# Optimization experiments

Hardware: AMD Instinct MI355X
Metric: run time of the kernel (lower is better)

The kernel has to match this reference:

```python
import jax, jax.numpy as jnp
import numpy as np

B, L, H, NH, NB = 8, 200, 128, 4, 2
HD = H // NH
ITEM_NUM, TIME_SPAN = 50000, 256
PAD = -2.0**32 + 1.0


def setup_inputs() -> dict:
    key = jax.random.key(0)
    ks = jax.random.split(key, 32)
    def g(i, shape, s=0.02):
        return jax.random.normal(ks[i], shape, jnp.float32) * s
    item_emb = g(0, (ITEM_NUM + 1, H)).at[0].set(0.0)  # padding_idx=0
    return dict(
        user_ids=jax.random.randint(ks[1], (B,), 0, 1000),
        log_seqs=jax.random.randint(ks[2], (B, L), 0, ITEM_NUM),
        time_matrices=jax.random.randint(ks[3], (B, L, L), 0, TIME_SPAN + 1),
        pos_seqs=jax.random.randint(ks[4], (B, L), 0, ITEM_NUM + 1),
        neg_seqs=jax.random.randint(ks[5], (B, L), 0, ITEM_NUM + 1),
        item_emb=item_emb,
        pos_K_emb=g(6, (L, H)), pos_V_emb=g(7, (L, H)),
        time_K_emb=g(8, (TIME_SPAN + 1, H)), time_V_emb=g(9, (TIME_SPAN + 1, H)),
        attn_ln_g=jnp.ones((NB, H)), attn_ln_b=jnp.zeros((NB, H)),
        Wq=g(10, (NB, H, H)), bq=jnp.zeros((NB, H)),
        Wk=g(11, (NB, H, H)), bk=jnp.zeros((NB, H)),
        Wv=g(12, (NB, H, H)), bv=jnp.zeros((NB, H)),
        fwd_ln_g=jnp.ones((NB, H)), fwd_ln_b=jnp.zeros((NB, H)),
        W1=g(13, (NB, H, H)), b1=jnp.zeros((NB, H)),
        W2=g(14, (NB, H, H)), b2=jnp.zeros((NB, H)),
        last_ln_g=jnp.ones((H,)), last_ln_b=jnp.zeros((H,)),
    )


def _ln(x, g, b, eps=1e-8):
    m = x.mean(-1, keepdims=True)
    v = jnp.var(x, axis=-1, keepdims=True)
    return (x - m) / jnp.sqrt(v + eps) * g + b


def _heads(x):
    # [..., H] -> [NH, ..., HD]; matches torch.cat(torch.split(x, HD, -1), 0)
    y = x.reshape(x.shape[:-1] + (NH, HD))
    return jnp.moveaxis(y, -2, 0)


def reference(user_ids, log_seqs, time_matrices, pos_seqs, neg_seqs, item_emb,
              pos_K_emb, pos_V_emb, time_K_emb, time_V_emb,
              attn_ln_g, attn_ln_b, Wq, bq, Wk, bk, Wv, bv,
              fwd_ln_g, fwd_ln_b, W1, b1, W2, b2, last_ln_g, last_ln_b):
    # user_ids is unused in the original forward as well.
    tmask = log_seqs == 0                                  # [B,L] True = pad
    keep = (~tmask)[..., None].astype(jnp.float32)
    seqs = item_emb[log_seqs] * np.float32(np.sqrt(H))
    seqs = seqs * keep
    pKh = _heads(pos_K_emb)                                # [NH,L,HD]
    pVh = _heads(pos_V_emb)
    tKh = _heads(time_K_emb[time_matrices])                # [NH,B,L,L,HD]
    tVh = _heads(time_V_emb[time_matrices])
    causal = ~jnp.tril(jnp.ones((L, L), bool))             # True above diag -> masked
    bad = tmask[:, :, None] | causal[None]                 # [B,L,L]
    scale = np.float32(np.sqrt(HD))
    for i in range(NB):
        Qin = _ln(seqs, attn_ln_g[i], attn_ln_b[i])
        Qh = _heads(Qin @ Wq[i].T + bq[i])                 # [NH,B,L,HD]
        Kh = _heads(seqs @ Wk[i].T + bk[i])
        Vh = _heads(seqs @ Wv[i].T + bv[i])
        attn = (jnp.einsum('nbqd,nbkd->nbqk', Qh, Kh)
                + jnp.einsum('nbqd,nkd->nbqk', Qh, pKh)
                + jnp.einsum('nbqkd,nbqd->nbqk', tKh, Qh)) / scale
        attn = jnp.where(bad[None], PAD, attn)
        attn = jax.nn.softmax(attn, axis=-1)
        out = (jnp.einsum('nbqk,nbkd->nbqd', attn, Vh)
               + jnp.einsum('nbqk,nkd->nbqd', attn, pVh)
               + jnp.einsum('nbqk,nbqkd->nbqd', attn, tVh))
        out = jnp.moveaxis(out, 0, -2).reshape(seqs.shape)  # merge heads -> [B,L,H]
        seqs = Qin + out                                    # residual uses LN'd Q (as in source)
        seqs = _ln(seqs, fwd_ln_g[i], fwd_ln_b[i])
        ff = jax.nn.relu(seqs @ W1[i].T + b1[i]) @ W2[i].T + b2[i] + seqs
        seqs = ff * keep
    log_feats = _ln(seqs, last_ln_g, last_ln_b)
    pos_logits = (log_feats * item_emb[pos_seqs]).sum(-1)   # [B,L]
    neg_logits = (log_feats * item_emb[neg_seqs]).sum(-1)
    return pos_logits, neg_logits
```

## Files before the change

kernel.cpp:

```cpp
#include <hip/hip_runtime.h>
#include <hip/hip_bf16.h>

#define BB 8
#define LL 200
#define HH 128
#define NHEAD 4
#define HDIM 32
#define NBLK 2
#define BL (BB * LL)
#define NT 257
#define QT 8
#define NQT 25
#define SSP 208
#define KTP 66
#define TSP 132

static constexpr float SQRT_H    = 11.313708498984761f;
static constexpr float INV_SCALE = 0.17677669529663687f;
static constexpr float PADV      = -4294967295.0f;

__global__ void k_qkv_gemm(const float* __restrict__ seqs_in,
                           const int* __restrict__ log_seqs,
                           const float* __restrict__ item_emb,
                           const float* __restrict__ g, const float* __restrict__ bia,
                           const float* __restrict__ Wq, const float* __restrict__ bq,
                           const float* __restrict__ Wk, const float* __restrict__ bk,
                           const float* __restrict__ Wv, const float* __restrict__ bv,
                           const float* __restrict__ posK, const float* __restrict__ posV,
                           float* __restrict__ Qin, float* __restrict__ Q,
                           float* __restrict__ K, float* __restrict__ V) {
    int mt = blockIdx.x / 24, nt = blockIdx.x % 24;
    int matsel = nt >> 3;
    int jb = (nt & 7) * 16;
    int row0 = mt * 32;
    int tid = threadIdx.x;
    __shared__ float As[32 * TSP];
    __shared__ float Bs[16 * TSP];

    {
        int r = tid >> 3, seg = tid & 7;
        int row = row0 + r;
        float4 vv[4];
        if (seqs_in) {
            #pragma unroll
            for (int i = 0; i < 4; i++)
                vv[i] = *(const float4*)(seqs_in + (size_t)row * HH + seg * 16 + i * 4);
        } else {
            int idx = log_seqs[row];
            if (idx == 0) {
                #pragma unroll
                for (int i = 0; i < 4; i++) vv[i] = make_float4(0.f, 0.f, 0.f, 0.f);
            } else {
                #pragma unroll
                for (int i = 0; i < 4; i++) {
                    float4 e = *(const float4*)(item_emb + (size_t)idx * HH + seg * 16 + i * 4);
                    vv[i] = make_float4(e.x * SQRT_H, e.y * SQRT_H, e.z * SQRT_H, e.w * SQRT_H);
                }
            }
        }
        if (matsel == 0) {
            float s = 0.f, s2 = 0.f;
            #pragma unroll
            for (int i = 0; i < 4; i++) {
                s  += vv[i].x + vv[i].y + vv[i].z + vv[i].w;
                s2 += vv[i].x * vv[i].x + vv[i].y * vv[i].y + vv[i].z * vv[i].z + vv[i].w * vv[i].w;
            }
            #pragma unroll
            for (int off = 1; off < 8; off <<= 1) {
                s  += __shfl_xor(s, off);
                s2 += __shfl_xor(s2, off);
            }
            float mean = s * (1.f / HH);
            float var  = s2 * (1.f / HH) - mean * mean;
            float inv  = 1.f / sqrtf(var + 1e-8f);
            #pragma unroll
            for (int i = 0; i < 4; i++) {
                int k = seg * 16 + i * 4;
                float4 g4 = *(const float4*)(g + k);
                float4 b4 = *(const float4*)(bia + k);
                float4 y;
                y.x = (vv[i].x - mean) * inv * g4.x + b4.x;
                y.y = (vv[i].y - mean) * inv * g4.y + b4.y;
                y.z = (vv[i].z - mean) * inv * g4.z + b4.z;
                y.w = (vv[i].w - mean) * inv * g4.w + b4.w;
                *(float4*)&As[r * TSP + k] = y;
                if (nt == 0) *(float4*)(Qin + (size_t)row * HH + k) = y;
            }
        } else {
            #pragma unroll
            for (int i = 0; i < 4; i++)
                *(float4*)&As[r * TSP + seg * 16 + i * 4] = vv[i];
        }
    }
    {
        const float* W = (matsel == 0) ? Wq : (matsel == 1) ? Wk : Wv;
        int j = tid >> 4, seg = tid & 15;
        float4 w = *(const float4*)(W + (size_t)(jb + j) * HH + seg * 8);
        float4 w2 = *(const float4*)(W + (size_t)(jb + j) * HH + seg * 8 + 4);
        *(float4*)&Bs[j * TSP + seg * 8] = w;
        *(float4*)&Bs[j * TSP + seg * 8 + 4] = w2;
    }
    __syncthreads();

    int m = tid >> 3, jg = tid & 7;
    float acc0 = 0.f, acc1 = 0.f;
    const float* ar = &As[m * TSP];
    const float* b0r = &Bs[(jg * 2) * TSP];
    const float* b1r = &Bs[(jg * 2 + 1) * TSP];
    #pragma unroll 4
    for (int k4 = 0; k4 < 32; k4++) {
        float4 a = *(const float4*)(ar + k4 * 4);
        float4 b0 = *(const float4*)(b0r + k4 * 4);
        float4 b1 = *(const float4*)(b1r + k4 * 4);
        acc0 += a.x * b0.x + a.y * b0.y + a.z * b0.z + a.w * b0.w;
        acc1 += a.x * b1.x + a.y * b1.y + a.z * b1.z + a.w * b1.w;
    }
    int row = row0 + m;
    int col = jb + jg * 2;
    int l = row % LL;
    if (matsel == 0) {
        float2 bb = *(const float2*)(bq + col);
        *(float2*)(Q + (size_t)row * HH + col) =
            make_float2((acc0 + bb.x) * INV_SCALE, (acc1 + bb.y) * INV_SCALE);
    } else if (matsel == 1) {
        float2 bb = *(const float2*)(bk + col);
        float2 pk = *(const float2*)(posK + (size_t)l * HH + col);
        *(float2*)(K + (size_t)row * HH + col) =
            make_float2(acc0 + bb.x + pk.x, acc1 + bb.y + pk.y);
    } else {
        float2 bb = *(const float2*)(bv + col);
        float2 pv = *(const float2*)(posV + (size_t)l * HH + col);
        *(float2*)(V + (size_t)row * HH + col) =
            make_float2(acc0 + bb.x + pv.x, acc1 + bb.y + pv.y);
    }
}

__global__ void k_attn(const float* __restrict__ Q, const float* __restrict__ K,
                       const float* __restrict__ V,
                       const float* __restrict__ timeK, const float* __restrict__ timeV,
                       const int* __restrict__ tm,
                       float* __restrict__ att) {
    int bn = blockIdx.x & 31;
    int b = bn >> 2, n = bn & 3;
    int qt = (NQT - 1) - (blockIdx.x >> 5);
    int q0 = qt * QT;
    int kmax = q0 + QT - 1;
    int tid = threadIdx.x;
    int wv = tid >> 6, ln = tid & 63;

    __shared__ float Qs[QT * HDIM];
    __shared__ float KstT[HDIM * KTP];
    __shared__ float DTW[QT * NT];
    __shared__ float Ssc[QT * SSP];
    __shared__ int   tmst[QT * LL];
    __shared__ float Ost[QT * HDIM];

    Ost[tid] = 0.f;
    if (tid < 64) {
        int qi = tid >> 3, d4 = tid & 7;
        *(float4*)(Qs + qi * HDIM + d4 * 4) =
            *(const float4*)(Q + ((size_t)(b * LL + q0 + qi)) * HH + n * HDIM + d4 * 4);
    }
    #pragma unroll
    for (int qi = 0; qi < QT; qi++)
        if (tid < LL)
            tmst[qi * LL + tid] = tm[((size_t)(b * LL + q0 + qi)) * LL + tid];
    __syncthreads();

    int k2 = tid & 31, qi_c = tid >> 5;

    for (int c = 0; c < 5; c++) {
        #pragma unroll
        for (int p = 0; p < 2; p++) {
            int idx = tid + p * 256;
            int r = idx >> 3, d4 = idx & 7;
            int tau = c * 64 + r;
            float4 w = make_float4(0.f, 0.f, 0.f, 0.f);
            if (tau < NT) w = *(const float4*)(timeK + (size_t)tau * HH + n * HDIM + d4 * 4);
            KstT[(d4 * 4 + 0) * KTP + r] = w.x;
            KstT[(d4 * 4 + 1) * KTP + r] = w.y;
            KstT[(d4 * 4 + 2) * KTP + r] = w.z;
            KstT[(d4 * 4 + 3) * KTP + r] = w.w;
        }
        __syncthreads();
        float a0 = 0.f, a1 = 0.f;
        #pragma unroll 4
        for (int d = 0; d < HDIM; d++) {
            float qv = Qs[qi_c * HDIM + d];
            float2 kv = *(const float2*)&KstT[d * KTP + k2 * 2];
            a0 += qv * kv.x; a1 += qv * kv.y;
        }
        int tau0 = c * 64 + k2 * 2;
        if (tau0 < NT)     DTW[qi_c * NT + tau0]     = a0;
        if (tau0 + 1 < NT) DTW[qi_c * NT + tau0 + 1] = a1;
        __syncthreads();
    }

    int nch = (kmax >> 6) + 1;
    for (int c = 0; c < nch; c++) {
        #pragma unroll
        for (int p = 0; p < 2; p++) {
            int idx = tid + p * 256;
            int r = idx >> 3, d4 = idx & 7;
            int k = c * 64 + r;
            float4 w = make_float4(0.f, 0.f, 0.f, 0.f);
            if (k < LL) w = *(const float4*)(K + ((size_t)(b * LL + k)) * HH + n * HDIM + d4 * 4);
            KstT[(d4 * 4 + 0) * KTP + r] = w.x;
            KstT[(d4 * 4 + 1) * KTP + r] = w.y;
            KstT[(d4 * 4 + 2) * KTP + r] = w.z;
            KstT[(d4 * 4 + 3) * KTP + r] = w.w;
        }
        __syncthreads();
        float a0 = 0.f, a1 = 0.f;
        #pragma unroll 4
        for (int d = 0; d < HDIM; d++) {
            float qv = Qs[qi_c * HDIM + d];
            float2 kv = *(const float2*)&KstT[d * KTP + k2 * 2];
            a0 += qv * kv.x; a1 += qv * kv.y;
        }
        int q = q0 + qi_c;
        int k0 = c * 64 + k2 * 2;
        if (k0 <= kmax)
            Ssc[qi_c * SSP + k0] = (k0 <= q) ? (a0 + DTW[qi_c * NT + tmst[qi_c * LL + k0]]) : PADV;
        if (k0 + 1 <= kmax)
            Ssc[qi_c * SSP + k0 + 1] = (k0 + 1 <= q) ? (a1 + DTW[qi_c * NT + tmst[qi_c * LL + k0 + 1]]) : PADV;
        __syncthreads();
    }

    for (int idx = tid; idx < QT * NT; idx += 256) DTW[idx] = 0.f;
    __syncthreads();

    for (int rr = 0; rr < 2; rr++) {
        int qi = wv + rr * 4;
        int q = q0 + qi;
        float sv[4];
        float m = PADV;
        #pragma unroll
        for (int jj = 0; jj < 4; jj++) {
            int k = ln + 64 * jj;
            sv[jj] = (k <= q) ? Ssc[qi * SSP + k] : PADV;
            m = fmaxf(m, sv[jj]);
        }
        for (int off = 32; off; off >>= 1) m = fmaxf(m, __shfl_xor(m, off));
        float sum = 0.f;
        #pragma unroll
        for (int jj = 0; jj < 4; jj++) {
            int k = ln + 64 * jj;
            sv[jj] = (k <= q) ? __expf(sv[jj] - m) : 0.f;
            sum += sv[jj];
        }
        for (int off = 32; off; off >>= 1) sum += __shfl_xor(sum, off);
        float inv = 1.f / sum;
        #pragma unroll
        for (int jj = 0; jj < 4; jj++) {
            int k = ln + 64 * jj;
            float p = sv[jj] * inv;
            if (k < SSP) Ssc[qi * SSP + k] = (k <= q) ? p : 0.f;
            if (k <= q) atomicAdd(&DTW[qi * NT + tmst[qi * LL + k]], p);
        }
    }
    __syncthreads();

    int d = tid & 31, kg = tid >> 5;
    float acc[QT] = {0,0,0,0,0,0,0,0};
    const float* vb = V + ((size_t)(b * LL)) * HH + n * HDIM + d;
    for (int k = kg; k <= kmax; k += 8) {
        float v = vb[(size_t)k * HH];
        #pragma unroll
        for (int qi = 0; qi < QT; qi++) acc[qi] += Ssc[qi * SSP + k] * v;
    }
    const float* tvb = timeV + n * HDIM + d;
    for (int t = kg; t < NT; t += 8) {
        float v = tvb[(size_t)t * HH];
        #pragma unroll
        for (int qi = 0; qi < QT; qi++) acc[qi] += DTW[qi * NT + t] * v;
    }
    #pragma unroll
    for (int qi = 0; qi < QT; qi++) atomicAdd(&Ost[qi * HDIM + d], acc[qi]);
    __syncthreads();
    {
        int qi = tid >> 5;
        att[((size_t)(b * LL + q0 + qi)) * HH + n * HDIM + (tid & 31)] = Ost[tid];
    }
}

__global__ void k_ff1(const float* __restrict__ Qin, const float* __restrict__ att,
                      const float* __restrict__ g, const float* __restrict__ bia,
                      const float* __restrict__ W1, const float* __restrict__ b1,
                      float* __restrict__ h1) {
    int mt = blockIdx.x >> 3, jb = (blockIdx.x & 7) * 16;
    int row0 = mt * 16;
    int tid = threadIdx.x;
    __shared__ float As[16 * TSP];
    __shared__ float Bs[16 * TSP];

    {
        int r = tid >> 4, seg = tid & 15;
        int row = row0 + r;
        float4 vv[2];
        #pragma unroll
        for (int i = 0; i < 2; i++) {
            int k = seg * 8 + i * 4;
            float4 q4 = *(const float4*)(Qin + (size_t)row * HH + k);
            float4 a4 = *(const float4*)(att + (size_t)row * HH + k);
            vv[i] = make_float4(q4.x + a4.x, q4.y + a4.y, q4.z + a4.z, q4.w + a4.w);
        }
        float s = 0.f, s2 = 0.f;
        #pragma unroll
        for (int i = 0; i < 2; i++) {
            s  += vv[i].x + vv[i].y + vv[i].z + vv[i].w;
            s2 += vv[i].x * vv[i].x + vv[i].y * vv[i].y + vv[i].z * vv[i].z + vv[i].w * vv[i].w;
        }
        #pragma unroll
        for (int off = 1; off < 16; off <<= 1) {
            s  += __shfl_xor(s, off);
            s2 += __shfl_xor(s2, off);
        }
        float mean = s * (1.f / HH);
        float var  = s2 * (1.f / HH) - mean * mean;
        float inv  = 1.f / sqrtf(var + 1e-8f);
        #pragma unroll
        for (int i = 0; i < 2; i++) {
            int k = seg * 8 + i * 4;
            float4 g4 = *(const float4*)(g + k);
            float4 b4 = *(const float4*)(bia + k);
            float4 y;
            y.x = (vv[i].x - mean) * inv * g4.x + b4.x;
            y.y = (vv[i].y - mean) * inv * g4.y + b4.y;
            y.z = (vv[i].z - mean) * inv * g4.z + b4.z;
            y.w = (vv[i].w - mean) * inv * g4.w + b4.w;
            *(float4*)&As[r * TSP + k] = y;
        }
    }
    {
        int j = tid >> 4, seg = tid & 15;
        *(float4*)&Bs[j * TSP + seg * 8]     = *(const float4*)(W1 + (size_t)(jb + j) * HH + seg * 8);
        *(float4*)&Bs[j * TSP + seg * 8 + 4] = *(const float4*)(W1 + (size_t)(jb + j) * HH + seg * 8 + 4);
    }
    __syncthreads();

    int m = tid >> 4, j = tid & 15;
    float acc = 0.f;
    const float* ar = &As[m * TSP];
    const float* br = &Bs[j * TSP];
    #pragma unroll 4
    for (int k4 = 0; k4 < 32; k4++) {
        float4 a = *(const float4*)(ar + k4 * 4);
        float4 b = *(const float4*)(br + k4 * 4);
        acc += a.x * b.x + a.y * b.y + a.z * b.z + a.w * b.w;
    }
    int col = jb + j;
    float t = acc + b1[col];
    h1[(size_t)(row0 + m) * HH + col] = t > 0.f ? t : 0.f;
}

__global__ void k_ff2(const float* __restrict__ h1,
                      const float* __restrict__ Qin, const float* __restrict__ att,
                      const float* __restrict__ g, const float* __restrict__ bia,
                      const float* __restrict__ W2, const float* __restrict__ b2,
                      const int* __restrict__ log_seqs,
                      float* __restrict__ out) {
    int mt = blockIdx.x >> 3, jb = (blockIdx.x & 7) * 16;
    int row0 = mt * 16;
    int tid = threadIdx.x;
    __shared__ float As[16 * TSP];
    __shared__ float Bs[16 * TSP];
    __shared__ float mu[16], rstd[16];

    {
        int r = tid >> 4, seg = tid & 15;
        int row = row0 + r;
        #pragma unroll
        for (int i = 0; i < 2; i++) {
            int k = seg * 8 + i * 4;
            *(float4*)&As[r * TSP + k] = *(const float4*)(h1 + (size_t)row * HH + k);
        }
        float s = 0.f, s2 = 0.f;
        #pragma unroll
        for (int i = 0; i < 2; i++) {
            int k = seg * 8 + i * 4;
            float4 q4 = *(const float4*)(Qin + (size_t)row * HH + k);
            float4 a4 = *(const float4*)(att + (size_t)row * HH + k);
            float4 v = make_float4(q4.x + a4.x, q4.y + a4.y, q4.z + a4.z, q4.w + a4.w);
            s  += v.x + v.y + v.z + v.w;
            s2 += v.x * v.x + v.y * v.y + v.z * v.z + v.w * v.w;
        }
        #pragma unroll
        for (int off = 1; off < 16; off <<= 1) {
            s  += __shfl_xor(s, off);
            s2 += __shfl_xor(s2, off);
        }
        float mean = s * (1.f / HH);
        float var  = s2 * (1.f / HH) - mean * mean;
        if (seg == 0) { mu[r] = mean; rstd[r] = 1.f / sqrtf(var + 1e-8f); }
    }
    {
        int j = tid >> 4, seg = tid & 15;
        *(float4*)&Bs[j * TSP + seg * 8]     = *(const float4*)(W2 + (size_t)(jb + j) * HH + seg * 8);
        *(float4*)&Bs[j * TSP + seg * 8 + 4] = *(const float4*)(W2 + (size_t)(jb + j) * HH + seg * 8 + 4);
    }
    __syncthreads();

    int m = tid >> 4, j = tid & 15;
    float acc = 0.f;
    const float* ar = &As[m * TSP];
    const float* br = &Bs[j * TSP];
    #pragma unroll 4
    for (int k4 = 0; k4 < 32; k4++) {
        float4 a = *(const float4*)(ar + k4 * 4);
        float4 b = *(const float4*)(br + k4 * 4);
        acc += a.x * b.x + a.y * b.y + a.z * b.z + a.w * b.w;
    }
    int row = row0 + m;
    int col = jb + j;
    float resid = Qin[(size_t)row * HH + col] + att[(size_t)row * HH + col];
    float y = (resid - mu[m]) * rstd[m] * g[col] + bia[col];
    float o = acc + b2[col] + y;
    if (log_seqs[row] == 0) o = 0.f;
    out[(size_t)row * HH + col] = o;
}

__global__ void k_lnlogits(const float* __restrict__ seqs,
                           const float* __restrict__ g, const float* __restrict__ bia,
                           const float* __restrict__ item_emb,
                           const int* __restrict__ pos, const int* __restrict__ neg,
                           float* __restrict__ out) {
    int row = blockIdx.x;
    int h = threadIdx.x;
    float v = seqs[(size_t)row * HH + h];
    float s = v, s2 = v * v;
    for (int off = 32; off; off >>= 1) {
        s  += __shfl_xor(s, off);
        s2 += __shfl_xor(s2, off);
    }
    __shared__ float r1[2], r2[2];
    if ((h & 63) == 0) { r1[h >> 6] = s; r2[h >> 6] = s2; }
    __syncthreads();
    float mean = (r1[0] + r1[1]) * (1.f / HH);
    float var  = (r2[0] + r2[1]) * (1.f / HH) - mean * mean;
    float inv = 1.f / sqrtf(var + 1e-8f);
    float f = (v - mean) * inv * g[h] + bia[h];

    int ip = pos[row], in_ = neg[row];
    float vp = f * item_emb[(size_t)ip * HH + h];
    float vn = f * item_emb[(size_t)in_ * HH + h];
    for (int off = 32; off; off >>= 1) {
        vp += __shfl_xor(vp, off);
        vn += __shfl_xor(vn, off);
    }
    __shared__ float rp[2], rn[2];
    if ((h & 63) == 0) { rp[h >> 6] = vp; rn[h >> 6] = vn; }
    __syncthreads();
    if (h == 0) {
        out[row]      = rp[0] + rp[1];
        out[BL + row] = rn[0] + rn[1];
    }
}

extern "C" void kernel_launch(void* const* d_in, const int* in_sizes, int n_in,
                              void* d_out, int out_size, void* d_ws, size_t ws_size,
                              hipStream_t stream) {
    const int* log_seqs   = (const int*)d_in[1];
    const int* tm         = (const int*)d_in[2];
    const int* pos_seqs   = (const int*)d_in[3];
    const int* neg_seqs   = (const int*)d_in[4];
    const float* item_emb = (const float*)d_in[5];
    const float* posK     = (const float*)d_in[6];
    const float* posV     = (const float*)d_in[7];
    const float* timeK    = (const float*)d_in[8];
    const float* timeV    = (const float*)d_in[9];
    const float* attn_g   = (const float*)d_in[10];
    const float* attn_b   = (const float*)d_in[11];
    const float* Wq       = (const float*)d_in[12];
    const float* bq       = (const float*)d_in[13];
    const float* Wk       = (const float*)d_in[14];
    const float* bk       = (const float*)d_in[15];
    const float* Wv       = (const float*)d_in[16];
    const float* bv       = (const float*)d_in[17];
    const float* fwd_g    = (const float*)d_in[18];
    const float* fwd_b    = (const float*)d_in[19];
    const float* W1       = (const float*)d_in[20];
    const float* b1       = (const float*)d_in[21];
    const float* W2       = (const float*)d_in[22];
    const float* b2       = (const float*)d_in[23];
    const float* last_g   = (const float*)d_in[24];
    const float* last_b   = (const float*)d_in[25];

    float* seqs = (float*)d_ws;
    float* Qin  = seqs + (size_t)BL * HH;
    float* Qb   = Qin  + (size_t)BL * HH;
    float* Kb   = Qb   + (size_t)BL * HH;
    float* Vb   = Kb   + (size_t)BL * HH;
    float* att  = Vb   + (size_t)BL * HH;
    float* h1   = att  + (size_t)BL * HH;

    for (int i = 0; i < NBLK; i++) {
        k_qkv_gemm<<<1200, 256, 0, stream>>>(i == 0 ? nullptr : seqs, log_seqs, item_emb,
                                             attn_g + i * HH, attn_b + i * HH,
                                             Wq + (size_t)i * HH * HH, bq + i * HH,
                                             Wk + (size_t)i * HH * HH, bk + i * HH,
                                             Wv + (size_t)i * HH * HH, bv + i * HH,
                                             posK, posV, Qin, Qb, Kb, Vb);
        k_attn<<<NQT * 32, 256, 0, stream>>>(Qb, Kb, Vb, timeK, timeV, tm, att);
        k_ff1<<<800, 256, 0, stream>>>(Qin, att, fwd_g + i * HH, fwd_b + i * HH,
                                       W1 + (size_t)i * HH * HH, b1 + i * HH, h1);
        k_ff2<<<800, 256, 0, stream>>>(h1, Qin, att, fwd_g + i * HH, fwd_b + i * HH,
                                       W2 + (size_t)i * HH * HH, b2 + i * HH,
                                       log_seqs, seqs);
    }
    k_lnlogits<<<BL, HH, 0, stream>>>(seqs, last_g, last_b, item_emb,
                                      pos_seqs, neg_seqs, (float*)d_out);
}
```

Baseline: 235.1 us.

## Fuse all stages into one persistent cooperative kernel with grid syncs

Replaces the nine separate kernel launches with a single persistent cooperative kernel that loops over tiles of each stage and separates stages with grid-wide barriers. Stage bodies become device functions sharing one static shared-memory buffer, and the final layernorm/logits stage handles two rows per block. The aim is to remove inter-kernel launch gaps and tail drain. The cost is grid-sync latency, a larger fixed shared-memory footprint that may limit occupancy, and grid-stride load imbalance (e.g. 1200 qkv tiles over a capped grid). The old multi-kernel path is kept as a fallback if the cooperative launch fails.

```diff
diff --git a/kernel.cpp b/kernel.cpp
--- a/kernel.cpp
+++ b/kernel.cpp
@@ -1,5 +1,7 @@
 #include <hip/hip_runtime.h>
-#include <hip/hip_bf16.h>
+#include <hip/hip_cooperative_groups.h>
+
+namespace cg = cooperative_groups;
 
 #define BB 8
 #define LL 200
@@ -19,23 +21,46 @@
 static constexpr float INV_SCALE = 0.17677669529663687f;
 static constexpr float PADV      = -4294967295.0f;
 
-__global__ void k_qkv_gemm(const float* __restrict__ seqs_in,
-                           const int* __restrict__ log_seqs,
-                           const float* __restrict__ item_emb,
-                           const float* __restrict__ g, const float* __restrict__ bia,
-                           const float* __restrict__ Wq, const float* __restrict__ bq,
-                           const float* __restrict__ Wk, const float* __restrict__ bk,
-                           const float* __restrict__ Wv, const float* __restrict__ bv,
-                           const float* __restrict__ posK, const float* __restrict__ posV,
-                           float* __restrict__ Qin, float* __restrict__ Q,
-                           float* __restrict__ K, float* __restrict__ V) {
-    int mt = blockIdx.x / 24, nt = blockIdx.x % 24;
+#define SMEM_WORDS 8192
+
+struct MegaArgs {
+    const int*   log_seqs;
+    const int*   tm;
+    const int*   pos_seqs;
+    const int*   neg_seqs;
+    const float* item_emb;
+    const float* posK;
+    const float* posV;
+    const float* timeK;
+    const float* timeV;
+    const float* attn_g; const float* attn_b;
+    const float* Wq; const float* bq;
+    const float* Wk; const float* bk;
+    const float* Wv; const float* bv;
+    const float* fwd_g; const float* fwd_b;
+    const float* W1; const float* b1;
+    const float* W2; const float* b2;
+    const float* last_g; const float* last_b;
+    float* seqs; float* Qin; float* Q; float* K; float* V; float* att; float* h1;
+    float* out;
+};
+
+__device__ __forceinline__ void qkv_tile(float* smem, int tile, int tid,
+        const float* seqs_in, const int* __restrict__ log_seqs,
+        const float* __restrict__ item_emb,
+        const float* __restrict__ g, const float* __restrict__ bia,
+        const float* __restrict__ Wq, const float* __restrict__ bq,
+        const float* __restrict__ Wk, const float* __restrict__ bk,
+        const float* __restrict__ Wv, const float* __restrict__ bv,
+        const float* __restrict__ posK, const float* __restrict__ posV,
+        float* __restrict__ Qin, float* __restrict__ Q,
+        float* __restrict__ K, float* __restrict__ V) {
+    float* As = smem;
+    float* Bs = smem + 32 * TSP;
+    int mt = tile / 24, nt = tile % 24;
     int matsel = nt >> 3;
     int jb = (nt & 7) * 16;
     int row0 = mt * 32;
-    int tid = threadIdx.x;
-    __shared__ float As[32 * TSP];
-    __shared__ float Bs[16 * TSP];
 
     {
         int r = tid >> 3, seg = tid & 7;
@@ -95,21 +120,21 @@
     {
         const float* W = (matsel == 0) ? Wq : (matsel == 1) ? Wk : Wv;
         int j = tid >> 4, seg = tid & 15;
-        float4 w = *(const float4*)(W + (size_t)(jb + j) * HH + seg * 8);
+        float4 w  = *(const float4*)(W + (size_t)(jb + j) * HH + seg * 8);
         float4 w2 = *(const float4*)(W + (size_t)(jb + j) * HH + seg * 8 + 4);
-        *(float4*)&Bs[j * TSP + seg * 8] = w;
+        *(float4*)&Bs[j * TSP + seg * 8]     = w;
         *(float4*)&Bs[j * TSP + seg * 8 + 4] = w2;
     }
     __syncthreads();
 
     int m = tid >> 3, jg = tid & 7;
     float acc0 = 0.f, acc1 = 0.f;
-    const float* ar = &As[m * TSP];
+    const float* ar  = &As[m * TSP];
     const float* b0r = &Bs[(jg * 2) * TSP];
     const float* b1r = &Bs[(jg * 2 + 1) * TSP];
     #pragma unroll 4
     for (int k4 = 0; k4 < 32; k4++) {
-        float4 a = *(const float4*)(ar + k4 * 4);
+        float4 a  = *(const float4*)(ar + k4 * 4);
         float4 b0 = *(const float4*)(b0r + k4 * 4);
         float4 b1 = *(const float4*)(b1r + k4 * 4);
         acc0 += a.x * b0.x + a.y * b0.y + a.z * b0.z + a.w * b0.w;
@@ -135,25 +160,24 @@
     }
 }
 
-__global__ void k_attn(const float* __restrict__ Q, const float* __restrict__ K,
-                       const float* __restrict__ V,
-                       const float* __restrict__ timeK, const float* __restrict__ timeV,
-                       const int* __restrict__ tm,
-                       float* __restrict__ att) {
-    int bn = blockIdx.x & 31;
+__device__ __forceinline__ void attn_tile(float* smem, int tile, int tid,
+        const float* __restrict__ Q, const float* __restrict__ K,
+        const float* __restrict__ V,
+        const float* __restrict__ timeK, const float* __restrict__ timeV,
+        const int* __restrict__ tm, float* __restrict__ att) {
+    float* Qs   = smem;
+    float* KstT = smem + 256;
+    float* DTW  = KstT + 2112;
+    float* Ssc  = DTW + 2056;
+    float* Ost  = Ssc + 1664;
+    int*   tmst = (int*)(Ost + 256);
+
+    int bn = tile & 31;
     int b = bn >> 2, n = bn & 3;
-    int qt = (NQT - 1) - (blockIdx.x >> 5);
+    int qt = (NQT - 1) - (tile >> 5);
     int q0 = qt * QT;
     int kmax = q0 + QT - 1;
-    int tid = threadIdx.x;
     int wv = tid >> 6, ln = tid & 63;
-
-    __shared__ float Qs[QT * HDIM];
-    __shared__ float KstT[HDIM * KTP];
-    __shared__ float DTW[QT * NT];
-    __shared__ float Ssc[QT * SSP];
-    __shared__ int   tmst[QT * LL];
-    __shared__ float Ost[QT * HDIM];
 
     Ost[tid] = 0.f;
     if (tid < 64) {
@@ -284,15 +308,15 @@
     }
 }
 
-__global__ void k_ff1(const float* __restrict__ Qin, const float* __restrict__ att,
-                      const float* __restrict__ g, const float* __restrict__ bia,
-                      const float* __restrict__ W1, const float* __restrict__ b1,
-                      float* __restrict__ h1) {
-    int mt = blockIdx.x >> 3, jb = (blockIdx.x & 7) * 16;
+__device__ __forceinline__ void ff1_tile(float* smem, int tile, int tid,
+        const float* __restrict__ Qin, const float* __restrict__ att,
+        const float* __restrict__ g, const float* __restrict__ bia,
+        const float* __restrict__ W1, const float* __restrict__ b1,
+        float* __restrict__ h1) {
+    float* As = smem;
+    float* Bs = smem + 16 * TSP;
+    int mt = tile >> 3, jb = (tile & 7) * 16;
     int row0 = mt * 16;
-    int tid = threadIdx.x;
-    __shared__ float As[16 * TSP];
-    __shared__ float Bs[16 * TSP];
 
     {
         int r = tid >> 4, seg = tid & 15;
@@ -354,18 +378,19 @@
     h1[(size_t)(row0 + m) * HH + col] = t > 0.f ? t : 0.f;
 }
 
-__global__ void k_ff2(const float* __restrict__ h1,
-                      const float* __restrict__ Qin, const float* __restrict__ att,
-                      const float* __restrict__ g, const float* __restrict__ bia,
-                      const float* __restrict__ W2, const float* __restrict__ b2,
-                      const int* __restrict__ log_seqs,
-                      float* __restrict__ out) {
-    int mt = blockIdx.x >> 3, jb = (blockIdx.x & 7) * 16;
+__device__ __forceinline__ void ff2_tile(float* smem, int tile, int tid,
+        const float* __restrict__ h1,
+        const float* __restrict__ Qin, const float* __restrict__ att,
+        const float* __restrict__ g, const float* __restrict__ bia,
+        const float* __restrict__ W2, const float* __restrict__ b2,
+        const int* __restrict__ log_seqs,
+        float* __restrict__ out) {
+    float* As   = smem;
+    float* Bs   = smem + 16 * TSP;
+    float* mu   = smem + 32 * TSP;
+    float* rstd = mu + 16;
+    int mt = tile >> 3, jb = (tile & 7) * 16;
     int row0 = mt * 16;
-    int tid = threadIdx.x;
-    __shared__ float As[16 * TSP];
-    __shared__ float Bs[16 * TSP];
-    __shared__ float mu[16], rstd[16];
 
     {
         int r = tid >> 4, seg = tid & 15;
@@ -420,24 +445,30 @@
     out[(size_t)row * HH + col] = o;
 }
 
-__global__ void k_lnlogits(const float* __restrict__ seqs,
-                           const float* __restrict__ g, const float* __restrict__ bia,
-                           const float* __restrict__ item_emb,
-                           const int* __restrict__ pos, const int* __restrict__ neg,
-                           float* __restrict__ out) {
-    int row = blockIdx.x;
-    int h = threadIdx.x;
+__device__ __forceinline__ void lnlog_pair(float* smem, int tile, int tid,
+        const float* __restrict__ seqs,
+        const float* __restrict__ g, const float* __restrict__ bia,
+        const float* __restrict__ item_emb,
+        const int* __restrict__ pos, const int* __restrict__ neg,
+        float* __restrict__ out) {
+    int row = tile * 2 + (tid >> 7);
+    int h = tid & 127;
     float v = seqs[(size_t)row * HH + h];
     float s = v, s2 = v * v;
     for (int off = 32; off; off >>= 1) {
         s  += __shfl_xor(s, off);
         s2 += __shfl_xor(s2, off);
     }
-    __shared__ float r1[2], r2[2];
-    if ((h & 63) == 0) { r1[h >> 6] = s; r2[h >> 6] = s2; }
-    __syncthreads();
-    float mean = (r1[0] + r1[1]) * (1.f / HH);
-    float var  = (r2[0] + r2[1]) * (1.f / HH) - mean * mean;
+    float* r1 = smem;
+    float* r2 = smem + 4;
+    float* rp = smem + 8;
+    float* rn = smem + 12;
+    int w = tid >> 6;
+    if ((tid & 63) == 0) { r1[w] = s; r2[w] = s2; }
+    __syncthreads();
+    int wb = (tid >> 7) << 1;
+    float mean = (r1[wb] + r1[wb + 1]) * (1.f / HH);
+    float var  = (r2[wb] + r2[wb + 1]) * (1.f / HH) - mean * mean;
     float inv = 1.f / sqrtf(var + 1e-8f);
     float f = (v - mean) * inv * g[h] + bia[h];
 
@@ -448,13 +479,87 @@
         vp += __shfl_xor(vp, off);
         vn += __shfl_xor(vn, off);
     }
-    __shared__ float rp[2], rn[2];
-    if ((h & 63) == 0) { rp[h >> 6] = vp; rn[h >> 6] = vn; }
-    __syncthreads();
-    if (h == 0) {
-        out[row]      = rp[0] + rp[1];
-        out[BL + row] = rn[0] + rn[1];
-    }
+    if ((tid & 63) == 0) { rp[w] = vp; rn[w] = vn; }
+    __syncthreads();
+    if ((tid & 127) == 0) {
+        out[row]      = rp[wb] + rp[wb + 1];
+        out[BL + row] = rn[wb] + rn[wb + 1];
+    }
+}
+
+__global__ __launch_bounds__(256, 4) void k_tisas_mega(MegaArgs p) {
+    cg::grid_group gg = cg::this_grid();
+    __shared__ __align__(16) float smem[SMEM_WORDS];
+    const int tid = threadIdx.x, bid = blockIdx.x, nb = gridDim.x;
+
+    for (int i = 0; i < NBLK; i++) {
+        const float* seqs_in = (i == 0) ? (const float*)nullptr : p.seqs;
+        for (int t = bid; t < 1200; t += nb) {
+            __syncthreads();
+            qkv_tile(smem, t, tid, seqs_in, p.log_seqs, p.item_emb,
+                     p.attn_g + i * HH, p.attn_b + i * HH,
+                     p.Wq + (size_t)i * HH * HH, p.bq + i * HH,
+                     p.Wk + (size_t)i * HH * HH, p.bk + i * HH,
+                     p.Wv + (size_t)i * HH * HH, p.bv + i * HH,
+                     p.posK, p.posV, p.Qin, p.Q, p.K, p.V);
+        }
+        gg.sync();
+        for (int t = bid; t < NQT * 32; t += nb) {
+            __syncthreads();
+            attn_tile(smem, t, tid, p.Q, p.K, p.V, p.timeK, p.timeV, p.tm, p.att);
+        }
+        gg.sync();
+        for (int t = bid; t < 800; t += nb) {
+            __syncthreads();
+            ff1_tile(smem, t, tid, p.Qin, p.att, p.fwd_g + i * HH, p.fwd_b + i * HH,
+                     p.W1 + (size_t)i * HH * HH, p.b1 + i * HH, p.h1);
+        }
+        gg.sync();
+        for (int t = bid; t < 800; t += nb) {
+            __syncthreads();
+            ff2_tile(smem, t, tid, p.h1, p.Qin, p.att, p.fwd_g + i * HH, p.fwd_b + i * HH,
+                     p.W2 + (size_t)i * HH * HH, p.b2 + i * HH, p.log_seqs, p.seqs);
+        }
+        gg.sync();
+    }
+    for (int t = bid; t < 800; t += nb) {
+        __syncthreads();
+        lnlog_pair(smem, t, tid, p.seqs, p.last_g, p.last_b, p.item_emb,
+                   p.pos_seqs, p.neg_seqs, p.out);
+    }
+}
+
+__global__ void k_qkv_gemm(const float* seqs_in, const int* log_seqs, const float* item_emb,
+                           const float* g, const float* bia,
+                           const float* Wq, const float* bq, const float* Wk, const float* bk,
+                           const float* Wv, const float* bv,
+                           const float* posK, const float* posV,
+                           float* Qin, float* Q, float* K, float* V) {
+    __shared__ __align__(16) float smem[48 * TSP];
+    qkv_tile(smem, blockIdx.x, threadIdx.x, seqs_in, log_seqs, item_emb, g, bia,
+             Wq, bq, Wk, bk, Wv, bv, posK, posV, Qin, Q, K, V);
+}
+__global__ void k_attn(const float* Q, const float* K, const float* V,
+                       const float* timeK, const float* timeV, const int* tm, float* att) {
+    __shared__ __align__(16) float smem[7944];
+    attn_tile(smem, blockIdx.x, threadIdx.x, Q, K, V, timeK, timeV, tm, att);
+}
+__global__ void k_ff1(const float* Qin, const float* att, const float* g, const float* bia,
+                      const float* W1, const float* b1, float* h1) {
+    __shared__ __align__(16) float smem[32 * TSP + 32];
+    ff1_tile(smem, blockIdx.x, threadIdx.x, Qin, att, g, bia, W1, b1, h1);
+}
+__global__ void k_ff2(const float* h1, const float* Qin, const float* att,
+                      const float* g, const float* bia, const float* W2, const float* b2,
+                      const int* log_seqs, float* out) {
+    __shared__ __align__(16) float smem[32 * TSP + 32];
+    ff2_tile(smem, blockIdx.x, threadIdx.x, h1, Qin, att, g, bia, W2, b2, log_seqs, out);
+}
+__global__ void k_lnlogits(const float* seqs, const float* g, const float* bia,
+                           const float* item_emb, const int* pos, const int* neg,
+                           float* out) {
+    __shared__ __align__(16) float smem[16];
+    lnlog_pair(smem, blockIdx.x, threadIdx.x, seqs, g, bia, item_emb, pos, neg, out);
 }
 
 extern "C" void kernel_launch(void* const* d_in, const int* in_sizes, int n_in,
@@ -494,20 +599,45 @@
     float* att  = Vb   + (size_t)BL * HH;
     float* h1   = att  + (size_t)BL * HH;
 
-    for (int i = 0; i < NBLK; i++) {
-        k_qkv_gemm<<<1200, 256, 0, stream>>>(i == 0 ? nullptr : seqs, log_seqs, item_emb,
-                                             attn_g + i * HH, attn_b + i * HH,
-                                             Wq + (size_t)i * HH * HH, bq + i * HH,
-                                             Wk + (size_t)i * HH * HH, bk + i * HH,
-                                             Wv + (size_t)i * HH * HH, bv + i * HH,
-                                             posK, posV, Qin, Qb, Kb, Vb);
-        k_attn<<<NQT * 32, 256, 0, stream>>>(Qb, Kb, Vb, timeK, timeV, tm, att);
-        k_ff1<<<800, 256, 0, stream>>>(Qin, att, fwd_g + i * HH, fwd_b + i * HH,
-                                       W1 + (size_t)i * HH * HH, b1 + i * HH, h1);
-        k_ff2<<<800, 256, 0, stream>>>(h1, Qin, att, fwd_g + i * HH, fwd_b + i * HH,
-                                       W2 + (size_t)i * HH * HH, b2 + i * HH,
-                                       log_seqs, seqs);
-    }
-    k_lnlogits<<<BL, HH, 0, stream>>>(seqs, last_g, last_b, item_emb,
-                                      pos_seqs, neg_seqs, (float*)d_out);
-}
+    MegaArgs a;
+    a.log_seqs = log_seqs; a.tm = tm; a.pos_seqs = pos_seqs; a.neg_seqs = neg_seqs;
+    a.item_emb = item_emb; a.posK = posK; a.posV = posV; a.timeK = timeK; a.timeV = timeV;
+    a.attn_g = attn_g; a.attn_b = attn_b;
+    a.Wq = Wq; a.bq = bq; a.Wk = Wk; a.bk = bk; a.Wv = Wv; a.bv = bv;
+    a.fwd_g = fwd_g; a.fwd_b = fwd_b; a.W1 = W1; a.b1 = b1; a.W2 = W2; a.b2 = b2;
+    a.last_g = last_g; a.last_b = last_b;
+    a.seqs = seqs; a.Qin = Qin; a.Q = Qb; a.K = Kb; a.V = Vb; a.att = att; a.h1 = h1;
+    a.out = (float*)d_out;
+
+    static int grid_sz = 0;
+    if (grid_sz == 0) {
+        int occ = 0;
+        if (hipOccupancyMaxActiveBlocksPerMultiprocessor(&occ, k_tisas_mega, 256, 0)
+                != hipSuccess || occ < 1)
+            occ = 2;
+        long gmax = (long)occ * 256;
+        grid_sz = (int)(gmax < 1024 ? gmax : 1024);
+    }
+
+    void* args[] = { (void*)&a };
+    hipError_t err = hipLaunchCooperativeKernel(k_tisas_mega, dim3(grid_sz), dim3(256),
+                                                args, 0, stream);
+    if (err != hipSuccess) {
+        for (int i = 0; i < NBLK; i++) {
+            k_qkv_gemm<<<1200, 256, 0, stream>>>(i == 0 ? nullptr : seqs, log_seqs, item_emb,
+                                                 attn_g + i * HH, attn_b + i * HH,
+                                                 Wq + (size_t)i * HH * HH, bq + i * HH,
+                                                 Wk + (size_t)i * HH * HH, bk + i * HH,
+                                                 Wv + (size_t)i * HH * HH, bv + i * HH,
+                                                 posK, posV, Qin, Qb, Kb, Vb);
+            k_attn<<<NQT * 32, 256, 0, stream>>>(Qb, Kb, Vb, timeK, timeV, tm, att);
+            k_ff1<<<800, 256, 0, stream>>>(Qin, att, fwd_g + i * HH, fwd_b + i * HH,
+                                           W1 + (size_t)i * HH * HH, b1 + i * HH, h1);
+            k_ff2<<<800, 256, 0, stream>>>(h1, Qin, att, fwd_g + i * HH, fwd_b + i * HH,
+                                           W2 + (size_t)i * HH * HH, b2 + i * HH,
+                                           log_seqs, seqs);
+        }
+        k_lnlogits<<<800, 256, 0, stream>>>(seqs, last_g, last_b, item_emb,
+                                            pos_seqs, neg_seqs, (float*)d_out);
+    }
+}
```

Result: slower. 751.3 us (+219.5%).

## Compute attention scores from register-held Q with direct global K loads

Applied to the files above, without the earlier changes.

The attention kernel no longer stages Q and transposed K/timeK tiles in shared memory, which needed many chunked loops and barriers. Each thread now keeps its query row in registers and reads key and time-key rows straight from global memory (relying on cache), computing only causal entries. This cuts the shared-memory transposes and syncs, but every thread re-reads K rows from global/L2 and uses more registers, and masked entries of Ssc are no longer written with PADV (softmax masks them separately).

```diff
diff --git a/kernel.cpp b/kernel.cpp
--- a/kernel.cpp
+++ b/kernel.cpp
@@ -1,5 +1,4 @@
 #include <hip/hip_runtime.h>
-#include <hip/hip_bf16.h>
 
 #define BB 8
 #define LL 200
@@ -12,7 +11,6 @@
 #define QT 8
 #define NQT 25
 #define SSP 208
-#define KTP 66
 #define TSP 132
 
 static constexpr float SQRT_H    = 11.313708498984761f;
@@ -95,21 +93,21 @@
     {
         const float* W = (matsel == 0) ? Wq : (matsel == 1) ? Wk : Wv;
         int j = tid >> 4, seg = tid & 15;
-        float4 w = *(const float4*)(W + (size_t)(jb + j) * HH + seg * 8);
+        float4 w  = *(const float4*)(W + (size_t)(jb + j) * HH + seg * 8);
         float4 w2 = *(const float4*)(W + (size_t)(jb + j) * HH + seg * 8 + 4);
-        *(float4*)&Bs[j * TSP + seg * 8] = w;
+        *(float4*)&Bs[j * TSP + seg * 8]     = w;
         *(float4*)&Bs[j * TSP + seg * 8 + 4] = w2;
     }
     __syncthreads();
 
     int m = tid >> 3, jg = tid & 7;
     float acc0 = 0.f, acc1 = 0.f;
-    const float* ar = &As[m * TSP];
+    const float* ar  = &As[m * TSP];
     const float* b0r = &Bs[(jg * 2) * TSP];
     const float* b1r = &Bs[(jg * 2 + 1) * TSP];
     #pragma unroll 4
     for (int k4 = 0; k4 < 32; k4++) {
-        float4 a = *(const float4*)(ar + k4 * 4);
+        float4 a  = *(const float4*)(ar + k4 * 4);
         float4 b0 = *(const float4*)(b0r + k4 * 4);
         float4 b1 = *(const float4*)(b1r + k4 * 4);
         acc0 += a.x * b0.x + a.y * b0.y + a.z * b0.z + a.w * b0.w;
@@ -148,97 +146,77 @@
     int tid = threadIdx.x;
     int wv = tid >> 6, ln = tid & 63;
 
-    __shared__ float Qs[QT * HDIM];
-    __shared__ float KstT[HDIM * KTP];
     __shared__ float DTW[QT * NT];
     __shared__ float Ssc[QT * SSP];
+    __shared__ float Ost[QT * HDIM];
     __shared__ int   tmst[QT * LL];
-    __shared__ float Ost[QT * HDIM];
-
-    Ost[tid] = 0.f;
-    if (tid < 64) {
-        int qi = tid >> 3, d4 = tid & 7;
-        *(float4*)(Qs + qi * HDIM + d4 * 4) =
-            *(const float4*)(Q + ((size_t)(b * LL + q0 + qi)) * HH + n * HDIM + d4 * 4);
-    }
+
     #pragma unroll
     for (int qi = 0; qi < QT; qi++)
         if (tid < LL)
             tmst[qi * LL + tid] = tm[((size_t)(b * LL + q0 + qi)) * LL + tid];
-    __syncthreads();
+    Ost[tid] = 0.f;
 
     int k2 = tid & 31, qi_c = tid >> 5;
-
-    for (int c = 0; c < 5; c++) {
-        #pragma unroll
-        for (int p = 0; p < 2; p++) {
-            int idx = tid + p * 256;
-            int r = idx >> 3, d4 = idx & 7;
-            int tau = c * 64 + r;
-            float4 w = make_float4(0.f, 0.f, 0.f, 0.f);
-            if (tau < NT) w = *(const float4*)(timeK + (size_t)tau * HH + n * HDIM + d4 * 4);
-            KstT[(d4 * 4 + 0) * KTP + r] = w.x;
-            KstT[(d4 * 4 + 1) * KTP + r] = w.y;
-            KstT[(d4 * 4 + 2) * KTP + r] = w.z;
-            KstT[(d4 * 4 + 3) * KTP + r] = w.w;
-        }
-        __syncthreads();
-        float a0 = 0.f, a1 = 0.f;
-        #pragma unroll 4
-        for (int d = 0; d < HDIM; d++) {
-            float qv = Qs[qi_c * HDIM + d];
-            float2 kv = *(const float2*)&KstT[d * KTP + k2 * 2];
-            a0 += qv * kv.x; a1 += qv * kv.y;
-        }
-        int tau0 = c * 64 + k2 * 2;
-        if (tau0 < NT)     DTW[qi_c * NT + tau0]     = a0;
-        if (tau0 + 1 < NT) DTW[qi_c * NT + tau0 + 1] = a1;
-        __syncthreads();
-    }
-
-    int nch = (kmax >> 6) + 1;
-    for (int c = 0; c < nch; c++) {
-        #pragma unroll
-        for (int p = 0; p < 2; p++) {
-            int idx = tid + p * 256;
-            int r = idx >> 3, d4 = idx & 7;
-            int k = c * 64 + r;
-            float4 w = make_float4(0.f, 0.f, 0.f, 0.f);
-            if (k < LL) w = *(const float4*)(K + ((size_t)(b * LL + k)) * HH + n * HDIM + d4 * 4);
-            KstT[(d4 * 4 + 0) * KTP + r] = w.x;
-            KstT[(d4 * 4 + 1) * KTP + r] = w.y;
-            KstT[(d4 * 4 + 2) * KTP + r] = w.z;
-            KstT[(d4 * 4 + 3) * KTP + r] = w.w;
-        }
-        __syncthreads();
-        float a0 = 0.f, a1 = 0.f;
-        #pragma unroll 4
-        for (int d = 0; d < HDIM; d++) {
-            float qv = Qs[qi_c * HDIM + d];
-            float2 kv = *(const float2*)&KstT[d * KTP + k2 * 2];
-            a0 += qv * kv.x; a1 += qv * kv.y;
-        }
-        int q = q0 + qi_c;
-        int k0 = c * 64 + k2 * 2;
-        if (k0 <= kmax)
-            Ssc[qi_c * SSP + k0] = (k0 <= q) ? (a0 + DTW[qi_c * NT + tmst[qi_c * LL + k0]]) : PADV;
-        if (k0 + 1 <= kmax)
-            Ssc[qi_c * SSP + k0 + 1] = (k0 + 1 <= q) ? (a1 + DTW[qi_c * NT + tmst[qi_c * LL + k0 + 1]]) : PADV;
-        __syncthreads();
-    }
+    int q = q0 + qi_c;
+
+    float qreg[HDIM];
+    {
+        const float* qp = Q + ((size_t)(b * LL + q)) * HH + n * HDIM;
+        #pragma unroll
+        for (int i = 0; i < 8; i++) {
+            float4 v = *(const float4*)(qp + i * 4);
+            qreg[i * 4 + 0] = v.x; qreg[i * 4 + 1] = v.y;
+            qreg[i * 4 + 2] = v.z; qreg[i * 4 + 3] = v.w;
+        }
+    }
+
+    #pragma unroll
+    for (int j = 0; j < 9; j++) {
+        int tau = k2 + 32 * j;
+        if (tau < NT) {
+            const float* tk = timeK + (size_t)tau * HH + n * HDIM;
+            float a = 0.f;
+            #pragma unroll
+            for (int i = 0; i < 8; i++) {
+                float4 w = *(const float4*)(tk + i * 4);
+                a += qreg[i * 4 + 0] * w.x + qreg[i * 4 + 1] * w.y
+                   + qreg[i * 4 + 2] * w.z + qreg[i * 4 + 3] * w.w;
+            }
+            DTW[qi_c * NT + tau] = a;
+        }
+    }
+    __syncthreads();
+
+    #pragma unroll
+    for (int j = 0; j < 7; j++) {
+        int k = k2 + 32 * j;
+        if (k <= q) {
+            const float* kp = K + ((size_t)(b * LL + k)) * HH + n * HDIM;
+            float a = 0.f;
+            #pragma unroll
+            for (int i = 0; i < 8; i++) {
+                float4 w = *(const float4*)(kp + i * 4);
+                a += qreg[i * 4 + 0] * w.x + qreg[i * 4 + 1] * w.y
+                   + qreg[i * 4 + 2] * w.z + qreg[i * 4 + 3] * w.w;
+            }
+            Ssc[qi_c * SSP + k] = a + DTW[qi_c * NT + tmst[qi_c * LL + k]];
+        }
+    }
+    __syncthreads();
 
     for (int idx = tid; idx < QT * NT; idx += 256) DTW[idx] = 0.f;
     __syncthreads();
 
     for (int rr = 0; rr < 2; rr++) {
         int qi = wv + rr * 4;
-        int q = q0 + qi;
+        int qq = q0 + qi;
         float sv[4];
         float m = PADV;
         #pragma unroll
         for (int jj = 0; jj < 4; jj++) {
             int k = ln + 64 * jj;
-            sv[jj] = (k <= q) ? Ssc[qi * SSP + k] : PADV;
+            sv[jj] = (k <= qq) ? Ssc[qi * SSP + k] : PADV;
             m = fmaxf(m, sv[jj]);
         }
         for (int off = 32; off; off >>= 1) m = fmaxf(m, __shfl_xor(m, off));
@@ -246,7 +224,7 @@
         #pragma unroll
         for (int jj = 0; jj < 4; jj++) {
             int k = ln + 64 * jj;
-            sv[jj] = (k <= q) ? __expf(sv[jj] - m) : 0.f;
+            sv[jj] = (k <= qq) ? __expf(sv[jj] - m) : 0.f;
             sum += sv[jj];
         }
         for (int off = 32; off; off >>= 1) sum += __shfl_xor(sum, off);
@@ -255,8 +233,8 @@
         for (int jj = 0; jj < 4; jj++) {
             int k = ln + 64 * jj;
             float p = sv[jj] * inv;
-            if (k < SSP) Ssc[qi * SSP + k] = (k <= q) ? p : 0.f;
-            if (k <= q) atomicAdd(&DTW[qi * NT + tmst[qi * LL + k]], p);
+            if (k < SSP) Ssc[qi * SSP + k] = (k <= qq) ? p : 0.f;
+            if (k <= qq) atomicAdd(&DTW[qi * NT + tmst[qi * LL + k]], p);
         }
     }
     __syncthreads();
```

After: 302.0 us. +28.5%, slower.
